# Optimization experiments

Measured on AMD Instinct MI355X. Metric: run time of the kernel, lower is better.

The kernel has to match this reference:

```python
import jax, jax.numpy as jnp
import numpy as np

RANK = 12
PLANE_RES = 192
OUT_DIM = 32
N_PTS = 2000000


def _sample_plane(plane, u, v):
    """Bilinear sample of plane [R,H,W] at normalized coords u (->W axis), v (->H axis).
    Matches F.grid_sample(mode='bilinear', padding_mode='border', align_corners=True)
    with grid = stack([u*2-1, v*2-1]). Returns [N, R]."""
    R, H, W = plane.shape
    # align_corners=True: unnormalized coord = (g+1)/2*(size-1) = u*(size-1);
    # border padding == clamp coordinate to valid range before interpolation.
    x = jnp.clip(u * (W - 1), 0.0, W - 1)  # [N]
    y = jnp.clip(v * (H - 1), 0.0, H - 1)  # [N]
    x0 = jnp.floor(x).astype(jnp.int32)
    y0 = jnp.floor(y).astype(jnp.int32)
    x1 = jnp.minimum(x0 + 1, W - 1)
    y1 = jnp.minimum(y0 + 1, H - 1)
    wx = x - x0.astype(x.dtype)  # [N]
    wy = y - y0.astype(y.dtype)
    # gather 4 corners: plane[:, yi, xi] -> [R, N]
    p00 = plane[:, y0, x0]
    p01 = plane[:, y0, x1]
    p10 = plane[:, y1, x0]
    p11 = plane[:, y1, x1]
    top = p00 * (1 - wx) + p01 * wx
    bot = p10 * (1 - wx) + p11 * wx
    out = top * (1 - wy) + bot * wy  # [R, N]
    return out.T  # [N, R]


def setup_inputs() -> dict:
    key = jax.random.key(0)
    k1, k2, k3, k4, k5 = jax.random.split(key, 5)
    xyz = jax.random.uniform(k1, (N_PTS, 3), dtype=jnp.float32)  # in [0,1]^3
    std = 0.3
    xy = std * jax.random.truncated_normal(k2, -2.0, 2.0, (RANK, PLANE_RES, PLANE_RES), dtype=jnp.float32)
    xz = std * jax.random.truncated_normal(k3, -2.0, 2.0, (RANK, PLANE_RES, PLANE_RES), dtype=jnp.float32)
    yz = std * jax.random.truncated_normal(k4, -2.0, 2.0, (RANK, PLANE_RES, PLANE_RES), dtype=jnp.float32)
    # xavier uniform for Linear(3*rank, out_dim, bias=False): weight [out_dim, 3*rank]
    fan_in, fan_out = 3 * RANK, OUT_DIM
    limit = float(np.sqrt(6.0 / (fan_in + fan_out)))
    w_mlp = jax.random.uniform(k5, (OUT_DIM, 3 * RANK), minval=-limit, maxval=limit, dtype=jnp.float32)
    return {"xyz": xyz, "xy": xy, "xz": xz, "yz": yz, "w_mlp": w_mlp}


def reference(xyz, xy, xz, yz, w_mlp):
    x, y, z = xyz[..., 0], xyz[..., 1], xyz[..., 2]
    f_xy = _sample_plane(xy, x, y)  # [N, R]
    f_xz = _sample_plane(xz, x, z)
    f_yz = _sample_plane(yz, y, z)
    f = jnp.concatenate([f_xy, f_xz, f_yz], axis=-1)  # [N, 3R]
    return f @ w_mlp.T  # [N, out_dim]
```

## Files before the change

kernel.cpp:

```cpp
#include <hip/hip_runtime.h>
#include <hip/hip_fp16.h>

#define RANK 12
#define RES 192
#define NHW (RES * RES)
#define NF 36
#define ODIM 32
#define TEXW 16
#define NB 4096
#define SORTB 256
#define SORTT 1024
#define TRB 108
#define LROW 36

typedef float f32x4 __attribute__((ext_vector_type(4)));
typedef _Float16 h2 __attribute__((ext_vector_type(2)));

__device__ __forceinline__ float fdot2(h2 a, h2 b, float c) {
#if __has_builtin(__builtin_amdgcn_fdot2)
    return __builtin_amdgcn_fdot2(a, b, c, false);
#else
    return c + (float)a.x * (float)b.x + (float)a.y * (float)b.y;
#endif
}

__device__ __forceinline__ int cell16(float x, float y, float z) {
    int qx = min(15, max(0, (int)(x * 16.0f)));
    int qy = min(15, max(0, (int)(y * 16.0f)));
    int qz = min(15, max(0, (int)(z * 16.0f)));
    return (qz << 8) | (qy << 4) | qx;
}

__global__ __launch_bounds__(SORTT) void vme_pre(const float* __restrict__ a,
                                                 const float* __restrict__ b,
                                                 const float* __restrict__ c,
                                                 const float* __restrict__ w,
                                                 _Float16* __restrict__ t,
                                                 unsigned* __restrict__ w2u,
                                                 const float* __restrict__ xyz,
                                                 int* __restrict__ m, int n) {
    if (blockIdx.x < TRB) {
        int idx = blockIdx.x * SORTT + threadIdx.x;
        if (idx < ODIM * NF / 2) {
            int o = idx / (NF / 2), k = idx - o * (NF / 2);
            union { h2 h; unsigned u; } cv;
            cv.h.x = (_Float16)w[o * NF + 2 * k];
            cv.h.y = (_Float16)w[o * NF + 2 * k + 1];
            w2u[idx] = cv.u;
        }
        if (idx >= 3 * NHW) return;
        int p = idx / NHW;
        int yx = idx - p * NHW;
        const float* src = (p == 0) ? a : (p == 1) ? b : c;
        _Float16* dst = t + (size_t)idx * TEXW;
#pragma unroll
        for (int r = 0; r < RANK; ++r) dst[r] = (_Float16)src[(size_t)r * NHW + yx];
#pragma unroll
        for (int r = RANK; r < TEXW; ++r) dst[r] = (_Float16)0.0f;
        return;
    }
    __shared__ int h[NB];
    int tt = threadIdx.x, bb = blockIdx.x - TRB;
    for (int k = tt; k < NB; k += SORTT) h[k] = 0;
    __syncthreads();
    int P = (n + SORTB - 1) / SORTB;
    int lo = bb * P, hi = min(n, lo + P);
    for (int i = lo + tt; i < hi; i += SORTT) {
        float x = xyz[3 * (size_t)i + 0];
        float y = xyz[3 * (size_t)i + 1];
        float z = xyz[3 * (size_t)i + 2];
        atomicAdd(&h[cell16(x, y, z)], 1);
    }
    __syncthreads();
    for (int k = tt; k < NB; k += SORTT) m[(size_t)bb * NB + k] = h[k];
}

__global__ __launch_bounds__(256) void vme_scan_cols(int* __restrict__ m,
                                                     int* __restrict__ T) {
    int k = blockIdx.x * 256 + threadIdx.x;
    int run = 0;
#pragma unroll 8
    for (int b = 0; b < SORTB; ++b) {
        size_t p = (size_t)b * NB + k;
        int v = m[p];
        m[p] = run;
        run += v;
    }
    T[k] = run;
}

__global__ __launch_bounds__(SORTT) void vme_scatter(const float* __restrict__ xyz,
                                                     const int* __restrict__ m,
                                                     const int* __restrict__ T,
                                                     f32x4* __restrict__ sorted, int n) {
    __shared__ int sT[NB];
    __shared__ int part[SORTT];
    __shared__ int bases[NB];
    __shared__ int ranks[NB];
    int t = threadIdx.x, b = blockIdx.x;

    {
        int base = t * (NB / SORTT);
        int l[NB / SORTT];
        int s = 0;
#pragma unroll
        for (int k = 0; k < NB / SORTT; ++k) { l[k] = T[base + k]; s += l[k]; }
        part[t] = s;
        __syncthreads();
        for (int off = 1; off < SORTT; off <<= 1) {
            int u = part[t];
            int add = (t >= off) ? part[t - off] : 0;
            __syncthreads();
            part[t] = u + add;
            __syncthreads();
        }
        int run = part[t] - s;
#pragma unroll
        for (int k = 0; k < NB / SORTT; ++k) { sT[base + k] = run; run += l[k]; }
    }
    __syncthreads();

    for (int k = t; k < NB; k += SORTT) {
        bases[k] = m[(size_t)b * NB + k] + sT[k];
        ranks[k] = 0;
    }
    __syncthreads();
    int P = (n + SORTB - 1) / SORTB;
    int lo = b * P, hi = min(n, lo + P);
    for (int i = lo + t; i < hi; i += SORTT) {
        float x = xyz[3 * (size_t)i + 0];
        float y = xyz[3 * (size_t)i + 1];
        float z = xyz[3 * (size_t)i + 2];
        int c = cell16(x, y, z);
        int r = atomicAdd(&ranks[c], 1);
        f32x4 v = {x, y, z, __uint_as_float((unsigned)i)};
        sorted[bases[c] + r] = v;
    }
}

__global__ __launch_bounds__(256) void vme_main_sorted(const f32x4* __restrict__ sorted,
                                                       const _Float16* __restrict__ tp,
                                                       const unsigned* __restrict__ w2u,
                                                       float* __restrict__ out, int n) {
    __shared__ float lrow[256 * LROW];
    __shared__ unsigned sidx[256];
    int tid = threadIdx.x;
    int j = blockIdx.x * 256 + tid;
    bool valid = j < n;

    float acc[ODIM];
#pragma unroll
    for (int o = 0; o < ODIM; ++o) acc[o] = 0.0f;
    unsigned idx = 0xFFFFFFFFu;

    if (valid) {
        f32x4 s = sorted[j];
        idx = __float_as_uint(s.w);
        float us[3] = {s.x, s.x, s.y};
        float vs[3] = {s.y, s.z, s.z};

        h2 f2[NF / 2];
#pragma unroll
        for (int p = 0; p < 3; ++p) {
            float x = us[p] * (float)(RES - 1);
            float y = vs[p] * (float)(RES - 1);
            x = fminf(fmaxf(x, 0.0f), (float)(RES - 1));
            y = fminf(fmaxf(y, 0.0f), (float)(RES - 1));
            int x0 = (int)x;
            int y0 = (int)y;
            int x1 = min(x0 + 1, RES - 1);
            int y1 = min(y0 + 1, RES - 1);
            float wx = x - (float)x0;
            float wy = y - (float)y0;
            _Float16 hw00 = (_Float16)((1.0f - wx) * (1.0f - wy));
            _Float16 hw01 = (_Float16)(wx * (1.0f - wy));
            _Float16 hw10 = (_Float16)((1.0f - wx) * wy);
            _Float16 hw11 = (_Float16)(wx * wy);
            h2 h00 = {hw00, hw00}, h01 = {hw01, hw01}, h10 = {hw10, hw10}, h11 = {hw11, hw11};

            const _Float16* base = tp + (size_t)p * NHW * TEXW;
            const _Float16* t00 = base + (size_t)(y0 * RES + x0) * TEXW;
            const _Float16* t01 = base + (size_t)(y0 * RES + x1) * TEXW;
            const _Float16* t10 = base + (size_t)(y1 * RES + x0) * TEXW;
            const _Float16* t11 = base + (size_t)(y1 * RES + x1) * TEXW;

            union TexA { uint4 v; h2 h[4]; } a00, a01, a10, a11;
            union TexB { uint2 v; h2 h[2]; } b00, b01, b10, b11;
            a00.v = *(const uint4*)(t00);  b00.v = *(const uint2*)(t00 + 8);
            a01.v = *(const uint4*)(t01);  b01.v = *(const uint2*)(t01 + 8);
            a10.v = *(const uint4*)(t10);  b10.v = *(const uint2*)(t10 + 8);
            a11.v = *(const uint4*)(t11);  b11.v = *(const uint2*)(t11 + 8);

#pragma unroll
            for (int q = 0; q < 4; ++q)
                f2[p * 6 + q] = a00.h[q] * h00 + a01.h[q] * h01 + a10.h[q] * h10 + a11.h[q] * h11;
#pragma unroll
            for (int q = 0; q < 2; ++q)
                f2[p * 6 + 4 + q] = b00.h[q] * h00 + b01.h[q] * h01 + b10.h[q] * h10 + b11.h[q] * h11;
        }

#pragma unroll
        for (int o = 0; o < ODIM; ++o) {
            float sum = 0.0f;
#pragma unroll
            for (int k = 0; k < NF / 2; ++k) {
                union { unsigned u; h2 h; } cv;
                cv.u = w2u[o * (NF / 2) + k];
                sum = fdot2(f2[k], cv.h, sum);
            }
            acc[o] = sum;
        }
    }

    sidx[tid] = idx;
#pragma unroll
    for (int q = 0; q < 8; ++q) {
        f32x4 v = {acc[4 * q + 0], acc[4 * q + 1], acc[4 * q + 2], acc[4 * q + 3]};
        *(f32x4*)&lrow[tid * LROW + 4 * q] = v;
    }
    __syncthreads();

    int c = tid & 7;
    int r0 = tid >> 3;
#pragma unroll
    for (int rr = 0; rr < 8; ++rr) {
        int r = r0 + rr * 32;
        unsigned id = sidx[r];
        if (id != 0xFFFFFFFFu) {
            f32x4 v = *(const f32x4*)&lrow[r * LROW + 4 * c];
            __builtin_nontemporal_store(v, (f32x4*)(out + (size_t)id * ODIM + 4 * c));
        }
    }
}

__global__ __launch_bounds__(256) void vme_transpose_only(const float* __restrict__ a,
                                                          const float* __restrict__ b,
                                                          const float* __restrict__ c,
                                                          _Float16* __restrict__ t) {
    int idx = blockIdx.x * 256 + threadIdx.x;
    if (idx >= 3 * NHW) return;
    int p = idx / NHW;
    int yx = idx - p * NHW;
    const float* src = (p == 0) ? a : (p == 1) ? b : c;
    _Float16* dst = t + (size_t)idx * TEXW;
#pragma unroll
    for (int r = 0; r < RANK; ++r) dst[r] = (_Float16)src[(size_t)r * NHW + yx];
#pragma unroll
    for (int r = RANK; r < TEXW; ++r) dst[r] = (_Float16)0.0f;
}

__device__ __forceinline__ void decode_texel(const _Float16* __restrict__ tex, float* __restrict__ o) {
    union { uint4 v; _Float16 h[8]; } A;
    union { uint2 v; _Float16 h[4]; } B;
    A.v = *(const uint4*)(tex);
    B.v = *(const uint2*)(tex + 8);
#pragma unroll
    for (int r = 0; r < 8; ++r) o[r] = (float)A.h[r];
#pragma unroll
    for (int r = 0; r < 4; ++r) o[8 + r] = (float)B.h[r];
}

__device__ __forceinline__ void vme_compute_point(float px, float py, float pz,
                                                  const _Float16* __restrict__ tp,
                                                  const float* __restrict__ w,
                                                  float* __restrict__ op) {
    float f[NF];
    float us[3] = {px, px, py};
    float vs[3] = {py, pz, pz};
#pragma unroll
    for (int p = 0; p < 3; ++p) {
        float x = us[p] * (float)(RES - 1);
        float y = vs[p] * (float)(RES - 1);
        x = fminf(fmaxf(x, 0.0f), (float)(RES - 1));
        y = fminf(fmaxf(y, 0.0f), (float)(RES - 1));
        int x0 = (int)x, y0 = (int)y;
        int x1 = min(x0 + 1, RES - 1), y1 = min(y0 + 1, RES - 1);
        float wx = x - (float)x0, wy = y - (float)y0;
        float w00 = (1.0f - wx) * (1.0f - wy), w01 = wx * (1.0f - wy);
        float w10 = (1.0f - wx) * wy, w11 = wx * wy;
        const _Float16* base = tp + (size_t)p * NHW * TEXW;
        float d00[RANK], d01[RANK], d10[RANK], d11[RANK];
        decode_texel(base + (size_t)(y0 * RES + x0) * TEXW, d00);
        decode_texel(base + (size_t)(y0 * RES + x1) * TEXW, d01);
        decode_texel(base + (size_t)(y1 * RES + x0) * TEXW, d10);
        decode_texel(base + (size_t)(y1 * RES + x1) * TEXW, d11);
#pragma unroll
        for (int r = 0; r < RANK; ++r)
            f[p * RANK + r] = w00 * d00[r] + w01 * d01[r] + w10 * d10[r] + w11 * d11[r];
    }
    float acc[ODIM];
#pragma unroll
    for (int o = 0; o < ODIM; ++o) {
        float s = 0.0f;
#pragma unroll
        for (int k = 0; k < NF; ++k) s += f[k] * w[o * NF + k];
        acc[o] = s;
    }
#pragma unroll
    for (int q = 0; q < 8; ++q) {
        f32x4 v = {acc[4 * q + 0], acc[4 * q + 1], acc[4 * q + 2], acc[4 * q + 3]};
        *(f32x4*)(op + 4 * q) = v;
    }
}

__global__ __launch_bounds__(256) void vme_main(const float* __restrict__ xyz,
                                                const _Float16* __restrict__ tp,
                                                const float* __restrict__ w,
                                                float* __restrict__ out, int n) {
    int i = blockIdx.x * 256 + threadIdx.x;
    if (i >= n) return;
    vme_compute_point(xyz[3 * (size_t)i], xyz[3 * (size_t)i + 1], xyz[3 * (size_t)i + 2],
                      tp, w, out + (size_t)i * ODIM);
}

__global__ __launch_bounds__(256) void vme_main_fb(const float* __restrict__ xyz,
                                                   const float* __restrict__ pa,
                                                   const float* __restrict__ pb,
                                                   const float* __restrict__ pc,
                                                   const float* __restrict__ w,
                                                   float* __restrict__ out, int n) {
    int i = blockIdx.x * 256 + threadIdx.x;
    if (i >= n) return;
    float px = xyz[3 * (size_t)i + 0];
    float py = xyz[3 * (size_t)i + 1];
    float pz = xyz[3 * (size_t)i + 2];
    float f[NF];
    float us[3] = {px, px, py};
    float vs[3] = {py, pz, pz};
#pragma unroll
    for (int p = 0; p < 3; ++p) {
        float x = us[p] * (float)(RES - 1);
        float y = vs[p] * (float)(RES - 1);
        x = fminf(fmaxf(x, 0.0f), (float)(RES - 1));
        y = fminf(fmaxf(y, 0.0f), (float)(RES - 1));
        int x0 = (int)x, y0 = (int)y;
        int x1 = min(x0 + 1, RES - 1), y1 = min(y0 + 1, RES - 1);
        float wx = x - (float)x0, wy = y - (float)y0;
        float w00 = (1.0f - wx) * (1.0f - wy), w01 = wx * (1.0f - wy);
        float w10 = (1.0f - wx) * wy, w11 = wx * wy;
        const float* base = (p == 0) ? pa : (p == 1) ? pb : pc;
        int i00 = y0 * RES + x0, i01 = y0 * RES + x1;
        int i10 = y1 * RES + x0, i11 = y1 * RES + x1;
#pragma unroll
        for (int r = 0; r < RANK; ++r) {
            const float* pr = base + (size_t)r * NHW;
            f[p * RANK + r] = w00 * pr[i00] + w01 * pr[i01] + w10 * pr[i10] + w11 * pr[i11];
        }
    }
    float acc[ODIM];
#pragma unroll
    for (int o = 0; o < ODIM; ++o) {
        float s = 0.0f;
#pragma unroll
        for (int k = 0; k < NF; ++k) s += f[k] * w[o * NF + k];
        acc[o] = s;
    }
    float4* op = (float4*)(out + (size_t)i * ODIM);
#pragma unroll
    for (int q = 0; q < 8; ++q)
        op[q] = make_float4(acc[4 * q], acc[4 * q + 1], acc[4 * q + 2], acc[4 * q + 3]);
}

extern "C" void kernel_launch(void* const* d_in, const int* in_sizes, int n_in,
                              void* d_out, int out_size, void* d_ws, size_t ws_size,
                              hipStream_t stream) {
    const float* xyz = (const float*)d_in[0];
    const float* xy  = (const float*)d_in[1];
    const float* xz  = (const float*)d_in[2];
    const float* yz  = (const float*)d_in[3];
    const float* wml = (const float*)d_in[4];
    float* out = (float*)d_out;

    int n = in_sizes[0] / 3;
    int nblk = (n + 255) / 256;
    int tblk = (3 * NHW + 255) / 256;

    const size_t TPB      = (size_t)3 * NHW * TEXW * sizeof(_Float16);
    const size_t OFF_W2   = TPB;
    const size_t OFF_HIST = TPB + 4096;
    const size_t OFF_T    = OFF_HIST + (size_t)NB * SORTB * 4;
    const size_t OFF_SORT = OFF_T + (size_t)NB * 4;
    const size_t WS_SORTED = OFF_SORT + (size_t)n * 16;

    char* ws = (char*)d_ws;

    if (d_ws && ws_size >= WS_SORTED) {
        _Float16* tp   = (_Float16*)(ws);
        unsigned* w2u  = (unsigned*)(ws + OFF_W2);
        int*      m    = (int*)(ws + OFF_HIST);
        int*      T    = (int*)(ws + OFF_T);
        f32x4*    srt  = (f32x4*)(ws + OFF_SORT);

        vme_pre<<<TRB + SORTB, SORTT, 0, stream>>>(xy, xz, yz, wml, tp, w2u, xyz, m, n);
        vme_scan_cols<<<NB / 256, 256, 0, stream>>>(m, T);
        vme_scatter<<<SORTB, SORTT, 0, stream>>>(xyz, m, T, srt, n);
        vme_main_sorted<<<nblk, 256, 0, stream>>>(srt, tp, w2u, out, n);
    } else if (d_ws && ws_size >= TPB) {
        _Float16* tp = (_Float16*)ws;
        vme_transpose_only<<<tblk, 256, 0, stream>>>(xy, xz, yz, tp);
        vme_main<<<nblk, 256, 0, stream>>>(xyz, tp, wml, out, n);
    } else {
        vme_main_fb<<<nblk, 256, 0, stream>>>(xyz, xy, xz, yz, wml, out, n);
    }
}
```

Measured before the change: 131.4 us.

## Shrink histogram to u16, halve LDS staging, add nontemporal loads

Stores the per-block cell histogram and its column prefix sums as 16-bit values instead of 32-bit, halving the traffic of the histogram and scan kernels. The main kernel's LDS output-staging buffer is halved by writing rows in two phases with extra barriers, and launch bounds request 6 blocks per CU, aiming for higher occupancy. Point and sorted-buffer reads use nontemporal loads. The u16 prefix overflows if a column's running count exceeds 65535 (about 2M/4096 ≈ 488 points per cell on uniform inputs, so it fits here), and the extra syncs add latency.

```diff
diff --git a/kernel.cpp b/kernel.cpp
--- a/kernel.cpp
+++ b/kernel.cpp
@@ -38,7 +38,7 @@
                                                  _Float16* __restrict__ t,
                                                  unsigned* __restrict__ w2u,
                                                  const float* __restrict__ xyz,
-                                                 int* __restrict__ m, int n) {
+                                                 unsigned short* __restrict__ m, int n) {
     if (blockIdx.x < TRB) {
         int idx = blockIdx.x * SORTT + threadIdx.x;
         if (idx < ODIM * NF / 2) {
@@ -66,31 +66,31 @@
     int P = (n + SORTB - 1) / SORTB;
     int lo = bb * P, hi = min(n, lo + P);
     for (int i = lo + tt; i < hi; i += SORTT) {
-        float x = xyz[3 * (size_t)i + 0];
-        float y = xyz[3 * (size_t)i + 1];
-        float z = xyz[3 * (size_t)i + 2];
+        float x = __builtin_nontemporal_load(xyz + 3 * (size_t)i + 0);
+        float y = __builtin_nontemporal_load(xyz + 3 * (size_t)i + 1);
+        float z = __builtin_nontemporal_load(xyz + 3 * (size_t)i + 2);
         atomicAdd(&h[cell16(x, y, z)], 1);
     }
     __syncthreads();
-    for (int k = tt; k < NB; k += SORTT) m[(size_t)bb * NB + k] = h[k];
-}
-
-__global__ __launch_bounds__(256) void vme_scan_cols(int* __restrict__ m,
+    for (int k = tt; k < NB; k += SORTT) m[(size_t)bb * NB + k] = (unsigned short)h[k];
+}
+
+__global__ __launch_bounds__(256) void vme_scan_cols(unsigned short* __restrict__ m,
                                                      int* __restrict__ T) {
     int k = blockIdx.x * 256 + threadIdx.x;
-    int run = 0;
+    unsigned run = 0;
 #pragma unroll 8
     for (int b = 0; b < SORTB; ++b) {
         size_t p = (size_t)b * NB + k;
-        int v = m[p];
-        m[p] = run;
+        unsigned v = m[p];
+        m[p] = (unsigned short)run;
         run += v;
     }
-    T[k] = run;
+    T[k] = (int)run;
 }
 
 __global__ __launch_bounds__(SORTT) void vme_scatter(const float* __restrict__ xyz,
-                                                     const int* __restrict__ m,
+                                                     const unsigned short* __restrict__ m,
                                                      const int* __restrict__ T,
                                                      f32x4* __restrict__ sorted, int n) {
     __shared__ int sT[NB];
@@ -121,16 +121,16 @@
     __syncthreads();
 
     for (int k = t; k < NB; k += SORTT) {
-        bases[k] = m[(size_t)b * NB + k] + sT[k];
+        bases[k] = (int)m[(size_t)b * NB + k] + sT[k];
         ranks[k] = 0;
     }
     __syncthreads();
     int P = (n + SORTB - 1) / SORTB;
     int lo = b * P, hi = min(n, lo + P);
     for (int i = lo + t; i < hi; i += SORTT) {
-        float x = xyz[3 * (size_t)i + 0];
-        float y = xyz[3 * (size_t)i + 1];
-        float z = xyz[3 * (size_t)i + 2];
+        float x = __builtin_nontemporal_load(xyz + 3 * (size_t)i + 0);
+        float y = __builtin_nontemporal_load(xyz + 3 * (size_t)i + 1);
+        float z = __builtin_nontemporal_load(xyz + 3 * (size_t)i + 2);
         int c = cell16(x, y, z);
         int r = atomicAdd(&ranks[c], 1);
         f32x4 v = {x, y, z, __uint_as_float((unsigned)i)};
@@ -138,11 +138,11 @@
     }
 }
 
-__global__ __launch_bounds__(256) void vme_main_sorted(const f32x4* __restrict__ sorted,
-                                                       const _Float16* __restrict__ tp,
-                                                       const unsigned* __restrict__ w2u,
-                                                       float* __restrict__ out, int n) {
-    __shared__ float lrow[256 * LROW];
+__global__ __launch_bounds__(256, 6) void vme_main_sorted(const f32x4* __restrict__ sorted,
+                                                          const _Float16* __restrict__ tp,
+                                                          const unsigned* __restrict__ w2u,
+                                                          float* __restrict__ out, int n) {
+    __shared__ float lrow[128 * LROW];
     __shared__ unsigned sidx[256];
     int tid = threadIdx.x;
     int j = blockIdx.x * 256 + tid;
@@ -154,7 +154,7 @@
     unsigned idx = 0xFFFFFFFFu;
 
     if (valid) {
-        f32x4 s = sorted[j];
+        f32x4 s = __builtin_nontemporal_load(sorted + j);
         idx = __float_as_uint(s.w);
         float us[3] = {s.x, s.x, s.y};
         float vs[3] = {s.y, s.z, s.z};
@@ -213,23 +213,31 @@
     }
 
     sidx[tid] = idx;
-#pragma unroll
-    for (int q = 0; q < 8; ++q) {
-        f32x4 v = {acc[4 * q + 0], acc[4 * q + 1], acc[4 * q + 2], acc[4 * q + 3]};
-        *(f32x4*)&lrow[tid * LROW + 4 * q] = v;
-    }
-    __syncthreads();
-
     int c = tid & 7;
-    int r0 = tid >> 3;
-#pragma unroll
-    for (int rr = 0; rr < 8; ++rr) {
-        int r = r0 + rr * 32;
-        unsigned id = sidx[r];
-        if (id != 0xFFFFFFFFu) {
-            f32x4 v = *(const f32x4*)&lrow[r * LROW + 4 * c];
-            __builtin_nontemporal_store(v, (f32x4*)(out + (size_t)id * ODIM + 4 * c));
-        }
+
+#pragma unroll
+    for (int ph = 0; ph < 2; ++ph) {
+        int rbase = ph * 128;
+        if ((tid >> 7) == ph) {
+            int lr = tid & 127;
+#pragma unroll
+            for (int q = 0; q < 8; ++q) {
+                f32x4 v = {acc[4 * q + 0], acc[4 * q + 1], acc[4 * q + 2], acc[4 * q + 3]};
+                *(f32x4*)&lrow[lr * LROW + 4 * q] = v;
+            }
+        }
+        __syncthreads();
+        int r0 = tid >> 3;
+#pragma unroll
+        for (int rr = 0; rr < 4; ++rr) {
+            int lr = r0 + rr * 32;
+            unsigned id = sidx[rbase + lr];
+            if (id != 0xFFFFFFFFu) {
+                f32x4 v = *(const f32x4*)&lrow[lr * LROW + 4 * c];
+                __builtin_nontemporal_store(v, (f32x4*)(out + (size_t)id * ODIM + 4 * c));
+            }
+        }
+        __syncthreads();
     }
 }
 
@@ -378,18 +386,18 @@
     const size_t TPB      = (size_t)3 * NHW * TEXW * sizeof(_Float16);
     const size_t OFF_W2   = TPB;
     const size_t OFF_HIST = TPB + 4096;
-    const size_t OFF_T    = OFF_HIST + (size_t)NB * SORTB * 4;
+    const size_t OFF_T    = OFF_HIST + (size_t)NB * SORTB * 2;
     const size_t OFF_SORT = OFF_T + (size_t)NB * 4;
     const size_t WS_SORTED = OFF_SORT + (size_t)n * 16;
 
     char* ws = (char*)d_ws;
 
     if (d_ws && ws_size >= WS_SORTED) {
-        _Float16* tp   = (_Float16*)(ws);
-        unsigned* w2u  = (unsigned*)(ws + OFF_W2);
-        int*      m    = (int*)(ws + OFF_HIST);
-        int*      T    = (int*)(ws + OFF_T);
-        f32x4*    srt  = (f32x4*)(ws + OFF_SORT);
+        _Float16*       tp  = (_Float16*)(ws);
+        unsigned*       w2u = (unsigned*)(ws + OFF_W2);
+        unsigned short* m   = (unsigned short*)(ws + OFF_HIST);
+        int*            T   = (int*)(ws + OFF_T);
+        f32x4*          srt = (f32x4*)(ws + OFF_SORT);
 
         vme_pre<<<TRB + SORTB, SORTT, 0, stream>>>(xy, xz, yz, wml, tp, w2u, xyz, m, n);
         vme_scan_cols<<<NB / 256, 256, 0, stream>>>(m, T);
```

Measured after the change: 150.7 us. 1.15x slower.
